# Kernel optimization log

Measured on AMD Instinct MI355X. Metric: run time of the kernel, lower is better.

Reference implementation:

```python
import jax, jax.numpy as jnp
import numpy as np

B, S, E, D = 4, 2048, 1024, 64  # batch, seq, embed_size, low-rank d; dv = E

def setup_inputs() -> dict:
    key = jax.random.key(0)
    ks = jax.random.split(key, 10)
    sc_e = 1.0 / np.sqrt(E)
    sc_d = 1.0 / np.sqrt(D)
    return {
        "x": jax.random.normal(ks[0], (B, S, E), jnp.float32),
        "y": jax.random.normal(ks[1], (B, S, E), jnp.float32),
        "Wq": jax.random.uniform(ks[2], (D, E), jnp.float32, -sc_e, sc_e),
        "bq": jax.random.uniform(ks[3], (D,), jnp.float32, -sc_e, sc_e),
        "Wk": jax.random.uniform(ks[4], (D, E), jnp.float32, -sc_e, sc_e),
        "bk": jax.random.uniform(ks[5], (D,), jnp.float32, -sc_e, sc_e),
        "WvR": jax.random.uniform(ks[6], (D, E), jnp.float32, -sc_e, sc_e),
        "bvR": jax.random.uniform(ks[7], (D,), jnp.float32, -sc_e, sc_e),
        "WvL": jax.random.uniform(ks[8], (E, D), jnp.float32, -sc_d, sc_d),
        "bvL": jax.random.uniform(ks[9], (E,), jnp.float32, -sc_d, sc_d),
    }

def reference(x, y, Wq, bq, Wk, bk, WvR, bvR, WvL, bvL):
    d = Wq.shape[0]
    Q = jnp.einsum('bse,de->bsd', x, Wq) + bq            # [B,S,D]
    K = jnp.einsum('bse,de->bsd', y, Wk) + bk            # [B,S,D]
    scores = jnp.einsum('bqd,bkd->bqk', Q, K) / jnp.sqrt(jnp.float32(d))
    # NOTE: original softmaxes over dim=1, i.e. the QUERY axis (faithful quirk)
    attn = jax.nn.softmax(scores, axis=1)                # [B,Sq,Sk]
    V = jnp.einsum('bsd,vd->bsv', jnp.einsum('bse,de->bsd', y, WvR) + bvR, WvL) + bvL  # [B,S,E]
    return jnp.einsum('bqk,bkv->bqv', attn, V)           # [B,S,E]
```

## Files before the change

kernel.cpp:

```cpp
#include <hip/hip_runtime.h>
#include <hip/hip_bf16.h>

#define DEV static __device__ __forceinline__
#define AS1 __attribute__((address_space(1)))
#define AS3 __attribute__((address_space(3)))

typedef __attribute__((ext_vector_type(8))) short bf16x8;
typedef __attribute__((ext_vector_type(4))) short bf16x4;
typedef __attribute__((ext_vector_type(4))) float f32x4;

constexpr int NB = 4;
constexpr int SS = 2048;
constexpr int EE = 1024;
constexpr int DD = 64;
constexpr int MTOT = NB * SS;

#define QSCALE (0.125f * 1.44269504088896340736f)

DEV short f2bf(float f) {
    union { float f; unsigned u; } v; v.f = f;
    unsigned u = v.u;
    u += 0x7FFFu + ((u >> 16) & 1u);
    return (short)(u >> 16);
}
DEV float bf2f(short h) {
    union { unsigned u; float f; } v; v.u = ((unsigned)(unsigned short)h) << 16;
    return v.f;
}
DEV unsigned pk2(float a, float b) {
    return (unsigned)(unsigned short)f2bf(a) | ((unsigned)(unsigned short)f2bf(b) << 16);
}

DEV bf16x8 load8(const float* p, float s) {
    float4 u = *(const float4*)(p);
    float4 v = *(const float4*)(p + 4);
    bf16x8 r;
    r[0] = f2bf(u.x * s); r[1] = f2bf(u.y * s); r[2] = f2bf(u.z * s); r[3] = f2bf(u.w * s);
    r[4] = f2bf(v.x * s); r[5] = f2bf(v.y * s); r[6] = f2bf(v.z * s); r[7] = f2bf(v.w * s);
    return r;
}

DEV f32x4 mfma16(bf16x8 a, bf16x8 b, f32x4 c) {
    return __builtin_amdgcn_mfma_f32_16x16x32_bf16(a, b, c, 0, 0, 0);
}

DEV float redmax16(float v) {
    v = fmaxf(v, __shfl_xor(v, 1)); v = fmaxf(v, __shfl_xor(v, 2));
    v = fmaxf(v, __shfl_xor(v, 4)); v = fmaxf(v, __shfl_xor(v, 8));
    return v;
}
DEV float redsum16(float v) {
    v += __shfl_xor(v, 1); v += __shfl_xor(v, 2);
    v += __shfl_xor(v, 4); v += __shfl_xor(v, 8);
    return v;
}


__global__ __launch_bounds__(256) void k_prep(
    const float* __restrict__ Wq, const float* __restrict__ Wk,
    const float* __restrict__ Wv, const float* __restrict__ WvL,
    const float* __restrict__ bvL,
    short* __restrict__ Wqb, short* __restrict__ Wkb, short* __restrict__ Wvb,
    short* __restrict__ Wcat2)
{
    int g = blockIdx.x * 256 + threadIdx.x;
    if (g < 24576) {
        int mat = g >> 13;
        int c = g & 8191;
        int lane = c & 63;
        int fn = (c >> 6) & 3;
        int it = (c >> 8) & 7;
        int kq4 = c >> 11;
        int r = lane & 15, half = lane >> 4;
        int row = fn * 16 + r;
        int col = kq4 * 256 + it * 32 + half * 8;
        const float* W = (mat == 0) ? Wq : ((mat == 1) ? Wk : Wv);
        short* O = (mat == 0) ? Wqb : ((mat == 1) ? Wkb : Wvb);
        float s = (mat == 0) ? QSCALE : 1.0f;
        bf16x8 o = load8(W + (size_t)row * EE + col, s);
        *(bf16x8*)(O + (size_t)c * 8) = o;
    } else {
        int i2 = g - 24576;
        int lane = i2 & 63;
        int ks = (i2 >> 6) % 5;
        int vt = i2 / 320;
        int r = lane & 15, h = lane >> 4;
        int v = vt * 16 + r;
        bf16x8 o;
        #pragma unroll
        for (int j = 0; j < 8; ++j) {
            int c = ks * 16 + (h & 1) * 8 + j;
            float val = (c < 64) ? WvL[(size_t)v * DD + c] : ((c == 64) ? bvL[v] : 0.f);
            o[j] = f2bf(val);
        }
        *(bf16x8*)(Wcat2 + ((size_t)(vt * 5 + ks) * 64 + lane) * 8) = o;
    }
}

__global__ __launch_bounds__(256) void k_proj(
    const float* __restrict__ x, const float* __restrict__ y,
    const short* __restrict__ Wqb, const short* __restrict__ Wkb,
    const short* __restrict__ Wvb,
    const float* __restrict__ bq, const float* __restrict__ bk,
    const float* __restrict__ bv,
    short* __restrict__ Qf, short* __restrict__ Kf, short* __restrict__ VF)
{
    const int tid = threadIdx.x, wave = tid >> 6, lane = tid & 63;
    const int r = lane & 15, half = lane >> 4;
    const int rb = blockIdx.x * 16;
    const bool isQ = (blockIdx.y == 0);
    const float* src = isQ ? x : y;
    const short* wA = isQ ? Wqb : Wkb;
    const int kq = wave * 256;

    __shared__ f32x4 red[4][8][64];

    f32x4 accA[4] = {}, accB[4] = {};
    const float* arow = src + (size_t)(rb + r) * EE + kq + half * 8;
    const short* wbase = wA + (size_t)wave * 16384 + lane * 8;
    const short* vbase = Wvb + (size_t)wave * 16384 + lane * 8;

    float4 af0[8], af1[8];
    #pragma unroll
    for (int it = 0; it < 8; ++it) {
        af0[it] = *(const float4*)(arow + it * 32);
        af1[it] = *(const float4*)(arow + it * 32 + 4);
    }

    #pragma unroll
    for (int it = 0; it < 8; ++it) {
        bf16x8 a;
        a[0] = f2bf(af0[it].x); a[1] = f2bf(af0[it].y);
        a[2] = f2bf(af0[it].z); a[3] = f2bf(af0[it].w);
        a[4] = f2bf(af1[it].x); a[5] = f2bf(af1[it].y);
        a[6] = f2bf(af1[it].z); a[7] = f2bf(af1[it].w);
        #pragma unroll
        for (int n = 0; n < 4; ++n) {
            bf16x8 b = *(const bf16x8*)(wbase + (it * 4 + n) * 64 * 8);
            accA[n] = mfma16(a, b, accA[n]);
        }
        if (!isQ) {
            #pragma unroll
            for (int n = 0; n < 4; ++n) {
                bf16x8 b = *(const bf16x8*)(vbase + (it * 4 + n) * 64 * 8);
                accB[n] = mfma16(a, b, accB[n]);
            }
        }
    }

    #pragma unroll
    for (int n = 0; n < 4; ++n) red[wave][n][lane] = accA[n];
    if (!isQ) {
        #pragma unroll
        for (int n = 0; n < 4; ++n) red[wave][4 + n][lane] = accB[n];
    }
    __syncthreads();

    const int n = wave;
    const int col = n * 16 + r;
    f32x4 s = red[0][n][lane];
    #pragma unroll
    for (int w = 1; w < 4; ++w) s += red[w][n][lane];
    float biasA = isQ ? (bq[col] * QSCALE) : bk[col];
    f32x4 t = {};
    float biasB = 0.f;
    if (!isQ) {
        t = red[0][4 + n][lane];
        #pragma unroll
        for (int w = 1; w < 4; ++w) t += red[w][4 + n][lane];
        biasB = bv[col];
    }
    __syncthreads();
    float* tlA = (float*)&red[0][0][0];
    float* tlB = tlA + 16 * 68;
    #pragma unroll
    for (int ri = 0; ri < 4; ++ri)
        tlA[(half * 4 + ri) * 68 + col] = s[ri] + biasA;
    if (!isQ) {
        #pragma unroll
        for (int ri = 0; ri < 4; ++ri)
            tlB[(half * 4 + ri) * 68 + col] = t[ri] + biasB;
    }
    __syncthreads();
    if (tid < 128) {
        int h2 = tid >> 6, l2 = tid & 63, r2 = l2 & 15, hh = l2 >> 4;
        bf16x8 o;
        #pragma unroll
        for (int j = 0; j < 8; ++j)
            o[j] = f2bf(tlA[r2 * 68 + h2 * 32 + hh * 8 + j]);
        short* dst = (isQ ? Qf : Kf) + ((size_t)blockIdx.x * 2 + h2) * 512 + l2 * 8;
        *(bf16x8*)dst = o;
    } else if (!isQ) {
        int idx = tid - 128;
        int nn = idx >> 5, sub = idx & 31;
        int r2 = sub & 15, su = sub >> 4;
        int hbase = (rb & 16) ? 2 : 0;
        int lane2 = ((hbase + su) << 4) | r2;
        bf16x8 o;
        #pragma unroll
        for (int j = 0; j < 8; ++j)
            o[j] = f2bf(tlB[(su * 8 + j) * 68 + nn * 16 + r2]);
        int batch = rb >> 11;
        int cg = (rb & 2047) >> 5;
        *(bf16x8*)(VF + (((size_t)batch * 64 + cg) * 4 + nn) * 512 + lane2 * 8) = o;
    }
}

__global__ __launch_bounds__(512) void k_stats(
    const short* __restrict__ Qf, const short* __restrict__ Kf,
    float* __restrict__ Ml, float* __restrict__ Rl)
{
    const int tid = threadIdx.x, wave = tid >> 6, lane = tid & 63;
    const int r = lane & 15, half = lane >> 4;
    const int batch = blockIdx.y;
    const int kb = blockIdx.x * 16;

    __shared__ float smax[8][16], ssum[8][16];

    const short* kfp = Kf + ((size_t)(batch * 128 + (kb >> 4)) * 2) * 512 + lane * 8;
    bf16x8 kf0 = *(const bf16x8*)kfp;
    bf16x8 kf1 = *(const bf16x8*)(kfp + 512);

    const int qt0 = batch * 128 + wave * 16;
    f32x4 s[16];
    #pragma unroll
    for (int t = 0; t < 16; ++t) {
        const short* qp = Qf + ((size_t)(qt0 + t) * 2) * 512 + lane * 8;
        bf16x8 a0 = *(const bf16x8*)qp;
        bf16x8 a1 = *(const bf16x8*)(qp + 512);
        f32x4 c = {};
        c = mfma16(kf0, a0, c);
        c = mfma16(kf1, a1, c);
        s[t] = c;
    }
    f32x4 m4 = s[0];
    #pragma unroll
    for (int t = 1; t < 16; ++t) {
        #pragma unroll
        for (int ri = 0; ri < 4; ++ri) m4[ri] = fmaxf(m4[ri], s[t][ri]);
    }
    #pragma unroll
    for (int ri = 0; ri < 4; ++ri) m4[ri] = redmax16(m4[ri]);
    if (r == 0) {
        #pragma unroll
        for (int ri = 0; ri < 4; ++ri) smax[wave][half * 4 + ri] = m4[ri];
    }
    __syncthreads();
    f32x4 M;
    #pragma unroll
    for (int ri = 0; ri < 4; ++ri) {
        float v = smax[0][half * 4 + ri];
        #pragma unroll
        for (int w = 1; w < 8; ++w) v = fmaxf(v, smax[w][half * 4 + ri]);
        M[ri] = v;
    }
    f32x4 l4 = {};
    #pragma unroll
    for (int t = 0; t < 16; ++t)
        #pragma unroll
        for (int ri = 0; ri < 4; ++ri) l4[ri] += exp2f(s[t][ri] - M[ri]);
    #pragma unroll
    for (int ri = 0; ri < 4; ++ri) l4[ri] = redsum16(l4[ri]);
    if (r == 0) {
        #pragma unroll
        for (int ri = 0; ri < 4; ++ri) ssum[wave][half * 4 + ri] = l4[ri];
    }
    __syncthreads();
    if (wave == 0 && r == 0) {
        f32x4 rl;
        #pragma unroll
        for (int ri = 0; ri < 4; ++ri) {
            float v = 0.f;
            #pragma unroll
            for (int w = 0; w < 8; ++w) v += ssum[w][half * 4 + ri];
            rl[ri] = 1.0f / v;
        }
        *(f32x4*)(Ml + (size_t)batch * SS + kb + half * 4) = M;
        *(f32x4*)(Rl + (size_t)batch * SS + kb + half * 4) = rl;
    }
}

__global__ __launch_bounds__(512) void k_pvfuse(
    const short* __restrict__ Qf, const short* __restrict__ Kf,
    const short* __restrict__ VF,
    const float* __restrict__ Ml, const float* __restrict__ Rl,
    short* __restrict__ Tcat2)
{
    const int tid = threadIdx.x, wave = tid >> 6, lane = tid & 63;
    const int r = lane & 15, half = lane >> 4;
    const int bid = blockIdx.x;
    const int qt = (bid & 7) * 64 + (bid >> 3);
    const int batch = qt >> 7;
    const int kbase = wave * 256;

    __shared__ short pl[8][16][40];
    __shared__ f32x4 red2[8][5][64];
    __shared__ float tl2[16][84];

    const short* qp = Qf + (size_t)qt * 2 * 512 + lane * 8;
    bf16x8 qf0 = *(const bf16x8*)qp;
    bf16x8 qf1 = *(const bf16x8*)(qp + 512);
    bf16x8 ones;
    #pragma unroll
    for (int j = 0; j < 8; ++j) ones[j] = (r == 0) ? (short)0x3F80 : (short)0;

    const float* mlb = Ml + (size_t)batch * SS;
    const float* rlb = Rl + (size_t)batch * SS;
    const short* kfb = Kf + (size_t)batch * 128 * 1024;
    const short* vfb = VF + (size_t)batch * 64 * 4 * 512;

    f32x4 acc[5] = {};

    #pragma unroll 2
    for (int st = 0; st < 8; ++st) {
        const int kt = kbase + st * 32;
        const short* kp = kfb + (size_t)(kt >> 4) * 1024 + lane * 8;
        bf16x8 k00 = *(const bf16x8*)kp;
        bf16x8 k01 = *(const bf16x8*)(kp + 512);
        bf16x8 k10 = *(const bf16x8*)(kp + 1024);
        bf16x8 k11 = *(const bf16x8*)(kp + 1536);
        f32x4 s0 = {}, s1 = {};
        s0 = mfma16(k00, qf0, s0); s0 = mfma16(k01, qf1, s0);
        s1 = mfma16(k10, qf0, s1); s1 = mfma16(k11, qf1, s1);
        f32x4 m0 = *(const f32x4*)(mlb + kt + half * 4);
        f32x4 r0 = *(const f32x4*)(rlb + kt + half * 4);
        f32x4 m1 = *(const f32x4*)(mlb + kt + 16 + half * 4);
        f32x4 r1 = *(const f32x4*)(rlb + kt + 16 + half * 4);
        f32x4 p0, p1;
        #pragma unroll
        for (int ri = 0; ri < 4; ++ri) {
            p0[ri] = exp2f(s0[ri] - m0[ri]) * r0[ri];
            p1[ri] = exp2f(s1[ri] - m1[ri]) * r1[ri];
        }
        uint2 u0, u1;
        u0.x = pk2(p0[0], p0[1]); u0.y = pk2(p0[2], p0[3]);
        u1.x = pk2(p1[0], p1[1]); u1.y = pk2(p1[2], p1[3]);
        *(uint2*)&pl[wave][r][4 * half] = u0;
        *(uint2*)&pl[wave][r][16 + 4 * half] = u1;
        bf16x8 af = *(const bf16x8*)&pl[wave][r][half * 8];
        #pragma unroll
        for (int nn = 0; nn < 4; ++nn) {
            bf16x8 vf = *(const bf16x8*)(vfb + ((size_t)(kt >> 5) * 4 + nn) * 512 + lane * 8);
            acc[nn] = mfma16(af, vf, acc[nn]);
        }
        acc[4] = mfma16(af, ones, acc[4]);
    }

    #pragma unroll
    for (int nn = 0; nn < 5; ++nn) red2[wave][nn][lane] = acc[nn];
    __syncthreads();
    if (wave < 5) {
        int nn = wave;
        f32x4 v = red2[0][nn][lane];
        #pragma unroll
        for (int w = 1; w < 8; ++w) v += red2[w][nn][lane];
        #pragma unroll
        for (int ri = 0; ri < 4; ++ri) tl2[half * 4 + ri][nn * 16 + r] = v[ri];
    }
    __syncthreads();
    if (tid < 320) {
        int ks = tid >> 6;
        int l2 = tid & 63;
        int r2 = l2 & 15, h2 = l2 >> 4;
        bf16x8 o;
        #pragma unroll
        for (int j = 0; j < 8; ++j) {
            float v = tl2[r2][ks * 16 + (h2 & 1) * 8 + j];
            short hi = f2bf(v);
            o[j] = (h2 < 2) ? hi : f2bf(v - bf2f(hi));
        }
        *(bf16x8*)(Tcat2 + (((size_t)qt * 5 + ks) * 64 + l2) * 8) = o;
    }
}

__global__ __launch_bounds__(256) void k_gemm2(
    const short* __restrict__ Tcat2, const short* __restrict__ Wcat2,
    float* __restrict__ out)
{
    const int tid = threadIdx.x, wave = tid >> 6, lane = tid & 63;
    const int r = lane & 15, half = lane >> 4;
    const int wm = wave >> 1, wn = wave & 1;
    const int bid = blockIdx.x;
    const int w = (bid & 7) * 64 + (bid >> 3);
    const int qB = (w >> 3) * 128;
    const int vB = (w & 7) * 128;
    const int tA0 = qB / 16 + wm * 4;
    const int vt0 = vB / 16 + wn * 4;

    f32x4 acc[4][4] = {};
    #pragma unroll
    for (int ks = 0; ks < 5; ++ks) {
        bf16x8 a[4], b[4];
        #pragma unroll
        for (int i = 0; i < 4; ++i) {
            a[i] = *(const bf16x8*)(Tcat2 + ((size_t)(tA0 + i) * 5 + ks) * 512 + lane * 8);
            b[i] = *(const bf16x8*)(Wcat2 + ((size_t)(vt0 + i) * 5 + ks) * 512 + lane * 8);
        }
        #pragma unroll
        for (int mi = 0; mi < 4; ++mi)
            #pragma unroll
            for (int ni = 0; ni < 4; ++ni)
                acc[mi][ni] = mfma16(a[mi], b[ni], acc[mi][ni]);
    }

    const int r4 = half * 4;
    #pragma unroll
    for (int mi = 0; mi < 4; ++mi)
        #pragma unroll
        for (int ni = 0; ni < 4; ++ni)
            #pragma unroll
            for (int ri = 0; ri < 4; ++ri)
                out[(size_t)(qB + wm * 64 + mi * 16 + r4 + ri) * EE + vB + wn * 64 + ni * 16 + r] = acc[mi][ni][ri];
}

extern "C" void kernel_launch(void* const* d_in, const int* in_sizes, int n_in,
                              void* d_out, int out_size, void* d_ws, size_t ws_size,
                              hipStream_t stream) {
    (void)in_sizes; (void)n_in; (void)out_size; (void)ws_size;
    const float* x   = (const float*)d_in[0];
    const float* y   = (const float*)d_in[1];
    const float* Wq  = (const float*)d_in[2];
    const float* bq  = (const float*)d_in[3];
    const float* Wk  = (const float*)d_in[4];
    const float* bk  = (const float*)d_in[5];
    const float* WvR = (const float*)d_in[6];
    const float* bvR = (const float*)d_in[7];
    const float* WvL = (const float*)d_in[8];
    const float* bvL = (const float*)d_in[9];
    float* out = (float*)d_out;

    short* Qf    = (short*)d_ws;
    short* Kf    = Qf    + (size_t)MTOT * DD;
    short* VF    = Kf    + (size_t)MTOT * DD;
    short* Tcat2 = VF    + (size_t)MTOT * DD;
    short* Wqb   = Tcat2 + (size_t)(MTOT / 16) * 5 * 512;
    short* Wkb   = Wqb   + (size_t)DD * EE;
    short* Wvb   = Wkb   + (size_t)DD * EE;
    short* Wcat2 = Wvb   + (size_t)DD * EE;
    float* Ml    = (float*)(Wcat2 + (size_t)64 * 5 * 512);
    float* Rl    = Ml + MTOT;

    k_prep<<<dim3(176), 256, 0, stream>>>(Wq, Wk, WvR, WvL, bvL, Wqb, Wkb, Wvb, Wcat2);
    k_proj<<<dim3(MTOT / 16, 2), 256, 0, stream>>>(x, y, Wqb, Wkb, Wvb, bq, bk, bvR, Qf, Kf, VF);
    k_stats<<<dim3(SS / 16, NB), 512, 0, stream>>>(Qf, Kf, Ml, Rl);
    k_pvfuse<<<dim3(512), 512, 0, stream>>>(Qf, Kf, VF, Ml, Rl, Tcat2);
    k_gemm2<<<dim3(512), 256, 0, stream>>>(Tcat2, Wcat2, out);
}
```

Baseline: 68.20 us.

## Fuse final low-rank output GEMM into the PV kernel epilogue

Merges the k_gemm2 launch into k_pvfuse. Each 512-thread block now turns its 16x80 reduced tile into bf16 hi/lo A-fragments in registers. Each of its 8 waves then computes 128 output columns directly against Wcat2. This removes the Tcat2 workspace round trip and one kernel launch. In exchange, Wcat2 is re-read by every block rather than reused across a 128x128 tile, and the output stores are done per 16-row tile.

```diff
diff --git a/kernel.cpp b/kernel.cpp
--- a/kernel.cpp
+++ b/kernel.cpp
@@ -280,11 +280,12 @@
     }
 }
 
-__global__ __launch_bounds__(512) void k_pvfuse(
+__global__ __launch_bounds__(512) void k_fused(
     const short* __restrict__ Qf, const short* __restrict__ Kf,
     const short* __restrict__ VF,
     const float* __restrict__ Ml, const float* __restrict__ Rl,
-    short* __restrict__ Tcat2)
+    const short* __restrict__ Wcat2,
+    float* __restrict__ out)
 {
     const int tid = threadIdx.x, wave = tid >> 6, lane = tid & 63;
     const int r = lane & 15, half = lane >> 4;
@@ -358,59 +359,38 @@
         for (int ri = 0; ri < 4; ++ri) tl2[half * 4 + ri][nn * 16 + r] = v[ri];
     }
     __syncthreads();
-    if (tid < 320) {
-        int ks = tid >> 6;
-        int l2 = tid & 63;
-        int r2 = l2 & 15, h2 = l2 >> 4;
+
+    bf16x8 afr[5];
+    #pragma unroll
+    for (int ks = 0; ks < 5; ++ks) {
         bf16x8 o;
         #pragma unroll
         for (int j = 0; j < 8; ++j) {
-            float v = tl2[r2][ks * 16 + (h2 & 1) * 8 + j];
+            float v = tl2[r][ks * 16 + (half & 1) * 8 + j];
             short hi = f2bf(v);
-            o[j] = (h2 < 2) ? hi : f2bf(v - bf2f(hi));
-        }
-        *(bf16x8*)(Tcat2 + (((size_t)qt * 5 + ks) * 64 + l2) * 8) = o;
-    }
-}
-
-__global__ __launch_bounds__(256) void k_gemm2(
-    const short* __restrict__ Tcat2, const short* __restrict__ Wcat2,
-    float* __restrict__ out)
-{
-    const int tid = threadIdx.x, wave = tid >> 6, lane = tid & 63;
-    const int r = lane & 15, half = lane >> 4;
-    const int wm = wave >> 1, wn = wave & 1;
-    const int bid = blockIdx.x;
-    const int w = (bid & 7) * 64 + (bid >> 3);
-    const int qB = (w >> 3) * 128;
-    const int vB = (w & 7) * 128;
-    const int tA0 = qB / 16 + wm * 4;
-    const int vt0 = vB / 16 + wn * 4;
-
-    f32x4 acc[4][4] = {};
-    #pragma unroll
-    for (int ks = 0; ks < 5; ++ks) {
-        bf16x8 a[4], b[4];
-        #pragma unroll
-        for (int i = 0; i < 4; ++i) {
-            a[i] = *(const bf16x8*)(Tcat2 + ((size_t)(tA0 + i) * 5 + ks) * 512 + lane * 8);
-            b[i] = *(const bf16x8*)(Wcat2 + ((size_t)(vt0 + i) * 5 + ks) * 512 + lane * 8);
-        }
-        #pragma unroll
-        for (int mi = 0; mi < 4; ++mi)
-            #pragma unroll
-            for (int ni = 0; ni < 4; ++ni)
-                acc[mi][ni] = mfma16(a[mi], b[ni], acc[mi][ni]);
-    }
-
+            o[j] = (half < 2) ? hi : f2bf(v - bf2f(hi));
+        }
+        afr[ks] = o;
+    }
+    f32x4 oacc[8];
+    #pragma unroll
+    for (int nn = 0; nn < 8; ++nn) {
+        int vt = wave * 8 + nn;
+        f32x4 a = {};
+        #pragma unroll
+        for (int ks = 0; ks < 5; ++ks) {
+            bf16x8 b = *(const bf16x8*)(Wcat2 + ((size_t)(vt * 5 + ks) * 64 + lane) * 8);
+            a = mfma16(afr[ks], b, a);
+        }
+        oacc[nn] = a;
+    }
+    float* op = out + (size_t)qt * 16 * EE + wave * 128;
     const int r4 = half * 4;
     #pragma unroll
-    for (int mi = 0; mi < 4; ++mi)
-        #pragma unroll
-        for (int ni = 0; ni < 4; ++ni)
-            #pragma unroll
-            for (int ri = 0; ri < 4; ++ri)
-                out[(size_t)(qB + wm * 64 + mi * 16 + r4 + ri) * EE + vB + wn * 64 + ni * 16 + r] = acc[mi][ni][ri];
+    for (int nn = 0; nn < 8; ++nn)
+        #pragma unroll
+        for (int ri = 0; ri < 4; ++ri)
+            op[(size_t)(r4 + ri) * EE + nn * 16 + r] = oacc[nn][ri];
 }
 
 extern "C" void kernel_launch(void* const* d_in, const int* in_sizes, int n_in,
@@ -432,8 +412,7 @@
     short* Qf    = (short*)d_ws;
     short* Kf    = Qf    + (size_t)MTOT * DD;
     short* VF    = Kf    + (size_t)MTOT * DD;
-    short* Tcat2 = VF    + (size_t)MTOT * DD;
-    short* Wqb   = Tcat2 + (size_t)(MTOT / 16) * 5 * 512;
+    short* Wqb   = VF    + (size_t)MTOT * DD;
     short* Wkb   = Wqb   + (size_t)DD * EE;
     short* Wvb   = Wkb   + (size_t)DD * EE;
     short* Wcat2 = Wvb   + (size_t)DD * EE;
@@ -443,6 +422,5 @@
     k_prep<<<dim3(176), 256, 0, stream>>>(Wq, Wk, WvR, WvL, bvL, Wqb, Wkb, Wvb, Wcat2);
     k_proj<<<dim3(MTOT / 16, 2), 256, 0, stream>>>(x, y, Wqb, Wkb, Wvb, bq, bk, bvR, Qf, Kf, VF);
     k_stats<<<dim3(SS / 16, NB), 512, 0, stream>>>(Qf, Kf, Ml, Rl);
-    k_pvfuse<<<dim3(512), 512, 0, stream>>>(Qf, Kf, VF, Ml, Rl, Tcat2);
-    k_gemm2<<<dim3(512), 256, 0, stream>>>(Tcat2, Wcat2, out);
-}
+    k_fused<<<dim3(512), 512, 0, stream>>>(Qf, Kf, VF, Ml, Rl, Wcat2, out);
+}
```

Result: slower. 70.63 us (+3.6%).
